# Kernel tuning notes

Measured on AMD Instinct MI355X. Metric: run time of the kernel, lower is better.

The kernel has to match this reference:

```python
import jax, jax.numpy as jnp
import numpy as np

N = 100000   # nodes
E = 1600000  # edges
IN, H1, H2, OUT = 512, 64, 16, 40


def setup_inputs() -> dict:
    key = jax.random.key(0)
    ks = jax.random.split(key, 8)
    x = jax.random.normal(ks[0], (N, IN), jnp.float32)
    edge_index = jax.random.randint(ks[1], (2, E), 0, N, dtype=jnp.int64)

    def glorot(k, i, o):
        s = np.sqrt(6.0 / (i + o)).astype(np.float32)
        return jax.random.uniform(k, (i, o), jnp.float32, -s, s)

    return dict(
        x=x, edge_index=edge_index,
        W1=glorot(ks[2], IN, H1), b1=jnp.zeros((H1,), jnp.float32),
        W2=glorot(ks[3], H1, H2), b2=jnp.zeros((H2,), jnp.float32),
        W3=glorot(ks[4], H2, OUT), b3=jnp.zeros((OUT,), jnp.float32),
    )


def _gcn_conv(x, src, dst, W, b):
    # PyG GCNConv: x' = D^{-1/2} (A + I) D^{-1/2} (x W) + b
    h = x @ W                                   # [N, F_out]
    n = x.shape[0]
    deg = jnp.zeros((n,), h.dtype).at[dst].add(1.0) + 1.0   # self-loop adds 1
    dinv = jax.lax.rsqrt(deg)                   # deg >= 1 always
    norm = dinv[src] * dinv[dst]                # [E]
    msg = h[src] * norm[:, None]                # gather + scale  [E, F_out]
    out = jnp.zeros_like(h).at[dst].add(msg)    # scatter-add to targets
    out = out + h * (dinv * dinv)[:, None]      # self-loop contribution
    return out + b


def reference(x, edge_index, W1, b1, W2, b2, W3, b3):
    src, dst = edge_index[0], edge_index[1]
    h = jax.nn.relu(_gcn_conv(x, src, dst, W1, b1))
    # dropout(p=0.2, training=False) -> identity
    h = jax.nn.relu(_gcn_conv(h, src, dst, W2, b2))
    h = _gcn_conv(h, src, dst, W3, b3)
    return jax.nn.log_softmax(h, axis=-1)
```

## Files before the change

### kernel.cpp

```cpp
#include <hip/hip_runtime.h>
#include <cstdint>
#include <cstddef>

#define NNODES 100000
#define NEDGES 1600000
#define NWIN 100
#define WIN_NODES 1000
#define WCAP 17408
#define WSTR 16

#define GM_ROWS 128
#define APAD 72
#define GEMM_BLOCKS ((NNODES + GM_ROWS - 1) / GM_ROWS)
#define BUCKET_BLOCKS 512
#define BCHUNK ((NEDGES + BUCKET_BLOCKS - 1) / BUCKET_BLOCKS)
#define MEGA_BLOCKS (GEMM_BLOCKS + BUCKET_BLOCKS)

typedef __attribute__((ext_vector_type(8))) short bf16x8;
typedef __attribute__((ext_vector_type(4))) float f32x4;
typedef __attribute__((ext_vector_type(4))) unsigned short ushort4v;
typedef __attribute__((ext_vector_type(8))) unsigned short ushort8v;

__device__ inline unsigned short f2bf(float f) {
    union { float f; unsigned u; } v; v.f = f;
    unsigned r = v.u + 0x7FFFu + ((v.u >> 16) & 1u);
    return (unsigned short)(r >> 16);
}
__device__ inline float bf2f(unsigned short b) {
    union { unsigned u; float f; } v; v.u = ((unsigned)b) << 16; return v.f;
}
__device__ inline void bfpair(unsigned u, float& lo, float& hi) {
    union { unsigned x; float f; } a, b;
    a.x = u << 16; b.x = u & 0xffff0000u;
    lo = a.f; hi = b.f;
}


__global__ __launch_bounds__(256) void convW(const float* __restrict__ W,
                                             unsigned short* __restrict__ Wt,
                                             int* __restrict__ wcur) {
    if (blockIdx.x == 0 && threadIdx.x < NWIN) wcur[threadIdx.x * WSTR] = 0;
    int i = blockIdx.x * 256 + threadIdx.x;
    if (i < 512 * 64) {
        int k = i >> 6, n = i & 63;
        Wt[n * 512 + k] = f2bf(W[i]);
    }
}


__global__ __launch_bounds__(256) void mega_gemm_bucket(
        const float* __restrict__ A,
        const unsigned short* __restrict__ Wt,
        unsigned short* __restrict__ Hs,
        const int* __restrict__ src, const int* __restrict__ dst,
        unsigned* __restrict__ stage,
        int* __restrict__ wcur, int M, int E) {
    __shared__ __align__(16) unsigned char smem[18432 + 9216];

    long long b = blockIdx.x;
    int g0 = (int)((b * GEMM_BLOCKS) / MEGA_BLOCKS);
    int g1 = (int)(((b + 1) * GEMM_BLOCKS) / MEGA_BLOCKS);

    if (g1 > g0) {
        typedef unsigned short RowA[APAD];
        RowA* As = (RowA*)smem;
        RowA* Bs = (RowA*)(smem + 18432);
        const int tid = threadIdx.x;
        const int wid = tid >> 6;
        const int lane = tid & 63;
        const int bm = g0 * GM_ROWS;

        f32x4 acc[2][4];
#pragma unroll
        for (int i = 0; i < 2; i++)
#pragma unroll
            for (int j = 0; j < 4; j++) acc[i][j] = (f32x4){0.f, 0.f, 0.f, 0.f};

        const int ar = tid >> 4;
        const int ac4 = tid & 15;
        const int lm = lane & 15;
        const int lk = (lane >> 4) * 8;

        float4 aR0[8], aR1[8];
        ushort8v bR0[2], bR1[2];

        auto LOADA = [&](float4 (&aRx)[8], ushort8v (&bRx)[2], int k0) {
#pragma unroll
            for (int p = 0; p < 8; p++) {
                int row = bm + p * 16 + ar;
                if (row < M) aRx[p] = *(const float4*)&A[(size_t)row * 512 + k0 + ac4 * 4];
                else         aRx[p] = make_float4(0.f, 0.f, 0.f, 0.f);
            }
#pragma unroll
            for (int p = 0; p < 2; p++) {
                int c = p * 256 + tid;
                int n = c >> 3, kc = c & 7;
                bRx[p] = *(const ushort8v*)&Wt[(size_t)n * 512 + k0 + kc * 8];
            }
        };

        auto TILE = [&](float4 (&aRx)[8], ushort8v (&bRx)[2], int k0) {
#pragma unroll
            for (int p = 0; p < 8; p++) {
                int r = p * 16 + ar;
                unsigned lo, hi;
                asm("v_cvt_pk_bf16_f32 %0, %1, %2" : "=v"(lo) : "v"(aRx[p].x), "v"(aRx[p].y));
                asm("v_cvt_pk_bf16_f32 %0, %1, %2" : "=v"(hi) : "v"(aRx[p].z), "v"(aRx[p].w));
                uint2 u; u.x = lo; u.y = hi;
                *(uint2*)&As[r][ac4 * 4] = u;
            }
#pragma unroll
            for (int p = 0; p < 2; p++) {
                int c = p * 256 + tid;
                int n = c >> 3, kc = c & 7;
                *(ushort8v*)&Bs[n][kc * 8] = bRx[p];
            }
            __syncthreads();

            if (k0 + 128 < 512) LOADA(aRx, bRx, k0 + 128);

            bf16x8 a[2][2], bb[4][2];
#pragma unroll
            for (int rf = 0; rf < 2; rf++)
#pragma unroll
                for (int kf = 0; kf < 2; kf++)
                    a[rf][kf] = *(const bf16x8*)&As[wid * 32 + rf * 16 + lm][kf * 32 + lk];
#pragma unroll
            for (int cf = 0; cf < 4; cf++)
#pragma unroll
                for (int kf = 0; kf < 2; kf++)
                    bb[cf][kf] = *(const bf16x8*)&Bs[cf * 16 + lm][kf * 32 + lk];

            __builtin_amdgcn_s_setprio(1);
#pragma unroll
            for (int kf = 0; kf < 2; kf++)
#pragma unroll
                for (int rf = 0; rf < 2; rf++)
#pragma unroll
                    for (int cf = 0; cf < 4; cf++)
                        acc[rf][cf] = __builtin_amdgcn_mfma_f32_16x16x32_bf16(
                            a[rf][kf], bb[cf][kf], acc[rf][cf], 0, 0, 0);
            __builtin_amdgcn_s_setprio(0);
            __syncthreads();
        };

        LOADA(aR0, bR0, 0);
        LOADA(aR1, bR1, 64);
        for (int tp = 0; tp < 4; tp++) {
            TILE(aR0, bR0, tp * 128);
            TILE(aR1, bR1, tp * 128 + 64);
        }

#pragma unroll
        for (int rf = 0; rf < 2; rf++) {
#pragma unroll
            for (int j = 0; j < 4; j++) {
                int row = bm + wid * 32 + rf * 16 + (lane >> 4) * 4 + j;
                if (row < M) {
#pragma unroll
                    for (int cf = 0; cf < 4; cf++)
                        Hs[(size_t)row * 64 + cf * 16 + lm] = f2bf(acc[rf][cf][j]);
                }
            }
        }
    } else {
        int bi = (int)(b - g0);
        int* cnt  = (int*)smem;
        int* lcur = cnt + NWIN;
        const int tid = threadIdx.x;
        int e0 = bi * BCHUNK;
        int e1 = e0 + BCHUNK; if (e1 > E) e1 = E;

        for (int i = tid; i < NWIN; i += 256) cnt[i] = 0;
        __syncthreads();
        for (int e = e0 + tid; e < e1; e += 256) {
            int d = dst[e];
            atomicAdd(&cnt[d / WIN_NODES], 1);
        }
        __syncthreads();
        for (int i = tid; i < NWIN; i += 256)
            lcur[i] = atomicAdd(&wcur[i * WSTR], cnt[i]);
        __syncthreads();
        for (int e = e0 + tid; e < e1; e += 256) {
            int d = dst[e], s = src[e];
            int w = d / WIN_NODES;
            int pos = atomicAdd(&lcur[w], 1);
            if (pos < WCAP)
                stage[(size_t)w * WCAP + pos] =
                    ((unsigned)(d - w * WIN_NODES) << 17) | (unsigned)s;
        }
    }
}


__global__ __launch_bounds__(256) void csr_window(
        const unsigned* __restrict__ stage,
        const int* __restrict__ wcur,
        int* __restrict__ rowstart,
        float* __restrict__ dinv,
        int* __restrict__ csr) {
    __shared__ int cnt[WIN_NODES];
    __shared__ int red[256];
    const int w = blockIdx.x;
    const int t = threadIdx.x;
    const int wb = w * WIN_NODES;
    const size_t sb = (size_t)w * WCAP;

    int v = (t < w) ? min(wcur[t * WSTR], WCAP) : 0;
    red[t] = v;
    __syncthreads();
#pragma unroll
    for (int off = 128; off > 0; off >>= 1) {
        if (t < off) red[t] += red[t + off];
        __syncthreads();
    }
    int woff = red[0];
    int n_w = min(wcur[w * WSTR], WCAP);
    __syncthreads();

    for (int i = t; i < WIN_NODES; i += 256) cnt[i] = 0;
    __syncthreads();
    for (int i = t; i < n_w; i += 256)
        atomicAdd(&cnt[stage[sb + i] >> 17], 1);
    __syncthreads();

    int c0 = 0, c1 = 0, c2 = 0, c3 = 0, psum = 0;
    if (t < 250) {
        c0 = cnt[4 * t]; c1 = cnt[4 * t + 1]; c2 = cnt[4 * t + 2]; c3 = cnt[4 * t + 3];
        psum = c0 + c1 + c2 + c3;
    }
    red[t] = psum;
    __syncthreads();
#pragma unroll
    for (int off = 1; off < 256; off <<= 1) {
        int tv = (t >= off) ? red[t - off] : 0;
        __syncthreads();
        red[t] += tv;
        __syncthreads();
    }
    int excl = red[t] - psum;
    if (t < 250) {
        int running = woff + excl;
        int idx = 4 * t;
        rowstart[wb + idx] = running; dinv[wb + idx] = rsqrtf((float)c0 + 1.f);
        cnt[idx] = running; running += c0;
        rowstart[wb + idx + 1] = running; dinv[wb + idx + 1] = rsqrtf((float)c1 + 1.f);
        cnt[idx + 1] = running; running += c1;
        rowstart[wb + idx + 2] = running; dinv[wb + idx + 2] = rsqrtf((float)c2 + 1.f);
        cnt[idx + 2] = running; running += c2;
        rowstart[wb + idx + 3] = running; dinv[wb + idx + 3] = rsqrtf((float)c3 + 1.f);
        cnt[idx + 3] = running;
    }
    if (w == NWIN - 1 && t == 0) rowstart[NNODES] = woff + n_w;
    __syncthreads();

    for (int i = t; i < n_w; i += 256) {
        unsigned p = stage[sb + i];
        int dl = (int)(p >> 17);
        int s  = (int)(p & 0x1FFFFu);
        int pos = atomicAdd(&cnt[dl], 1);
        csr[pos] = s;
    }
}


__global__ __launch_bounds__(256) void gather64_l2(
        const int* __restrict__ rowstart, const int* __restrict__ csr,
        const float* __restrict__ dinv,
        const unsigned short* __restrict__ Hs1,
        const float* __restrict__ b1,
        const float* __restrict__ W2,
        unsigned short* __restrict__ Hs2,
        int M) {
    __shared__ float Ws2[64 * 16];
    __shared__ float b1s[64];
    __shared__ float srow[8][64];
    for (int i = threadIdx.x; i < 64 * 16; i += 256) Ws2[i] = W2[i];
    if (threadIdx.x < 64) b1s[threadIdx.x] = b1[threadIdx.x];
    __syncthreads();

    const int r = threadIdx.x >> 5;
    const int lf = threadIdx.x & 31;
    const int row = blockIdx.x * 8 + r;
    const bool rok = (row < M);

    float v0 = 0.f, v1 = 0.f;
    if (rok) {
        const unsigned* H32 = (const unsigned*)Hs1;
        int e0 = rowstart[row], e1 = rowstart[row + 1];
        float dd = dinv[row];
        float acc0, acc1;
        bfpair(H32[(size_t)row * 32 + lf], acc0, acc1);
        acc0 *= dd; acc1 *= dd;
        int e = e0;
        for (; e + 3 < e1; e += 4) {
            int s0 = csr[e], s1 = csr[e + 1], s2 = csr[e + 2], s3 = csr[e + 3];
            float w0 = dinv[s0], w1 = dinv[s1], w2 = dinv[s2], w3 = dinv[s3];
            unsigned u0 = H32[(size_t)s0 * 32 + lf];
            unsigned u1 = H32[(size_t)s1 * 32 + lf];
            unsigned u2 = H32[(size_t)s2 * 32 + lf];
            unsigned u3 = H32[(size_t)s3 * 32 + lf];
            float a, b;
            bfpair(u0, a, b); acc0 += w0 * a; acc1 += w0 * b;
            bfpair(u1, a, b); acc0 += w1 * a; acc1 += w1 * b;
            bfpair(u2, a, b); acc0 += w2 * a; acc1 += w2 * b;
            bfpair(u3, a, b); acc0 += w3 * a; acc1 += w3 * b;
        }
        for (; e < e1; e++) {
            int s0 = csr[e];
            float w0 = dinv[s0];
            unsigned u = H32[(size_t)s0 * 32 + lf];
            float a, b;
            bfpair(u, a, b); acc0 += w0 * a; acc1 += w0 * b;
        }
        v0 = fmaxf(acc0 * dd + b1s[2 * lf], 0.f);
        v1 = fmaxf(acc1 * dd + b1s[2 * lf + 1], 0.f);
    }
    float2 t2; t2.x = v0; t2.y = v1;
    *(float2*)&srow[r][2 * lf] = t2;
    __syncthreads();

    if (rok && lf < 16) {
        float acc = 0.f;
#pragma unroll
        for (int k4 = 0; k4 < 16; k4++) {
            float4 s4 = *(const float4*)&srow[r][k4 * 4];
            acc += s4.x * Ws2[(k4 * 4 + 0) * 16 + lf];
            acc += s4.y * Ws2[(k4 * 4 + 1) * 16 + lf];
            acc += s4.z * Ws2[(k4 * 4 + 2) * 16 + lf];
            acc += s4.w * Ws2[(k4 * 4 + 3) * 16 + lf];
        }
        acc *= dinv[row];
        float hi = __shfl_down(acc, 1, 64);
        if ((lf & 1) == 0) {
            unsigned p = (unsigned)f2bf(acc) | ((unsigned)f2bf(hi) << 16);
            ((unsigned*)Hs2)[(size_t)row * 8 + (lf >> 1)] = p;
        }
    }
}


template <int F, bool RELU, bool SCALEOUT, bool HASBIAS, bool OUTBF>
__global__ __launch_bounds__(256) void gather_bf(
        const int* __restrict__ rowstart,
        const int* __restrict__ csr,
        const float* __restrict__ dinv,
        const unsigned short* __restrict__ Hs,
        const float* __restrict__ bias,
        void* __restrict__ outp,
        int M) {
    constexpr int LANES = F / 2;
    constexpr int GP = 256 / LANES;
    int row = blockIdx.x * GP + threadIdx.x / LANES;
    int lf = threadIdx.x % LANES;
    if (row >= M) return;

    const unsigned* H32 = (const unsigned*)Hs;
    const size_t LP = F / 2;

    int e0 = rowstart[row], e1 = rowstart[row + 1];
    float acc0, acc1;
    bfpair(H32[(size_t)row * LP + lf], acc0, acc1);

    int e = e0;
    for (; e + 3 < e1; e += 4) {
        int s0 = csr[e], s1 = csr[e + 1], s2 = csr[e + 2], s3 = csr[e + 3];
        unsigned u0 = H32[(size_t)s0 * LP + lf];
        unsigned u1 = H32[(size_t)s1 * LP + lf];
        unsigned u2 = H32[(size_t)s2 * LP + lf];
        unsigned u3 = H32[(size_t)s3 * LP + lf];
        float a, b;
        bfpair(u0, a, b); acc0 += a; acc1 += b;
        bfpair(u1, a, b); acc0 += a; acc1 += b;
        bfpair(u2, a, b); acc0 += a; acc1 += b;
        bfpair(u3, a, b); acc0 += a; acc1 += b;
    }
    for (; e < e1; e++) {
        unsigned u = H32[(size_t)csr[e] * LP + lf];
        float a, b;
        bfpair(u, a, b); acc0 += a; acc1 += b;
    }

    float dd = dinv[row];
    float v0 = acc0 * dd, v1 = acc1 * dd;
    if (HASBIAS) { v0 += bias[2 * lf]; v1 += bias[2 * lf + 1]; }
    if (RELU) { v0 = fmaxf(v0, 0.f); v1 = fmaxf(v1, 0.f); }
    if (SCALEOUT) { v0 *= dd; v1 *= dd; }
    if (OUTBF) {
        unsigned p = (unsigned)f2bf(v0) | ((unsigned)f2bf(v1) << 16);
        ((unsigned*)outp)[(size_t)row * LP + lf] = p;
    } else {
        float2 t; t.x = v0; t.y = v1;
        ((float2*)outp)[(size_t)row * LP + lf] = t;
    }
}


#define SRP 20

__global__ __launch_bounds__(256) void gather16_final(
        const int* __restrict__ rowstart, const int* __restrict__ csr,
        const float* __restrict__ dinv,
        const unsigned short* __restrict__ r2s,
        const float* __restrict__ W3,
        const float* __restrict__ b3,
        float* __restrict__ out,
        int M) {
    __shared__ float Ws3[16 * 40];
    __shared__ float bs3[40];
    __shared__ float srow[32][SRP];
    __shared__ float orow[32 * 40];
    for (int i = threadIdx.x; i < 16 * 40; i += 256) Ws3[i] = W3[i];
    if (threadIdx.x < 40) bs3[threadIdx.x] = b3[threadIdx.x];

    const int r = threadIdx.x >> 3;
    const int lf = threadIdx.x & 7;
    const int row = blockIdx.x * 32 + r;
    const bool rok = (row < M);

    float g0 = 0.f, g1 = 0.f;
    if (rok) {
        const unsigned* H32 = (const unsigned*)r2s;
        int e0 = rowstart[row], e1 = rowstart[row + 1];
        float acc0, acc1;
        bfpair(H32[(size_t)row * 8 + lf], acc0, acc1);
        int e = e0;
        for (; e + 3 < e1; e += 4) {
            int s0 = csr[e], s1 = csr[e + 1], s2 = csr[e + 2], s3 = csr[e + 3];
            unsigned u0 = H32[(size_t)s0 * 8 + lf];
            unsigned u1 = H32[(size_t)s1 * 8 + lf];
            unsigned u2 = H32[(size_t)s2 * 8 + lf];
            unsigned u3 = H32[(size_t)s3 * 8 + lf];
            float a, b;
            bfpair(u0, a, b); acc0 += a; acc1 += b;
            bfpair(u1, a, b); acc0 += a; acc1 += b;
            bfpair(u2, a, b); acc0 += a; acc1 += b;
            bfpair(u3, a, b); acc0 += a; acc1 += b;
        }
        for (; e < e1; e++) {
            unsigned u = H32[(size_t)csr[e] * 8 + lf];
            float a, b;
            bfpair(u, a, b); acc0 += a; acc1 += b;
        }
        float dd = dinv[row];
        g0 = acc0 * dd; g1 = acc1 * dd;
    }
    float2 t2; t2.x = g0; t2.y = g1;
    *(float2*)&srow[r][2 * lf] = t2;
    __syncthreads();

    float vals[5];
#pragma unroll
    for (int q = 0; q < 5; q++) vals[q] = bs3[lf + 8 * q];
#pragma unroll
    for (int k4 = 0; k4 < 4; k4++) {
        float4 s4 = *(const float4*)&srow[r][k4 * 4];
#pragma unroll
        for (int q = 0; q < 5; q++) {
            int n = lf + 8 * q;
            vals[q] += s4.x * Ws3[(k4 * 4 + 0) * 40 + n];
            vals[q] += s4.y * Ws3[(k4 * 4 + 1) * 40 + n];
            vals[q] += s4.z * Ws3[(k4 * 4 + 2) * 40 + n];
            vals[q] += s4.w * Ws3[(k4 * 4 + 3) * 40 + n];
        }
    }
    float m = vals[0];
#pragma unroll
    for (int q = 1; q < 5; q++) m = fmaxf(m, vals[q]);
#pragma unroll
    for (int off = 1; off < 8; off <<= 1) m = fmaxf(m, __shfl_xor(m, off, 64));
    float s = 0.f;
#pragma unroll
    for (int q = 0; q < 5; q++) s += expf(vals[q] - m);
#pragma unroll
    for (int off = 1; off < 8; off <<= 1) s += __shfl_xor(s, off, 64);
    float ls = logf(s) + m;
#pragma unroll
    for (int q = 0; q < 5; q++) orow[r * 40 + lf + 8 * q] = vals[q] - ls;
    __syncthreads();

    float4* o4 = (float4*)(out + (size_t)blockIdx.x * 32 * 40);
    const float4* s4p = (const float4*)orow;
    for (int i = threadIdx.x; i < 320; i += 256) {
        int rr = (i * 4) / 40;
        if (blockIdx.x * 32 + rr < M) o4[i] = s4p[i];
    }
}


extern "C" void kernel_launch(void* const* d_in, const int* in_sizes, int n_in,
                              void* d_out, int out_size, void* d_ws, size_t ws_size,
                              hipStream_t stream) {
    const float* x   = (const float*)d_in[0];
    const int*   ei  = (const int*)d_in[1];
    const int*   src = ei;
    const int*   dst = ei + NEDGES;
    const float* W1 = (const float*)d_in[2];
    const float* b1 = (const float*)d_in[3];
    const float* W2 = (const float*)d_in[4];
    const float* b2 = (const float*)d_in[5];
    const float* W3 = (const float*)d_in[6];
    const float* b3 = (const float*)d_in[7];
    float* out = (float*)d_out;

    int* ws_i = (int*)d_ws;
    int* wcur     = ws_i;
    int* rowstart = wcur + NWIN * WSTR + 16;
    int* csr      = rowstart + NNODES + 8;
    unsigned* stage = (unsigned*)(csr + NEDGES);
    float* dinv   = (float*)(stage + (size_t)NWIN * WCAP);
    unsigned short* Wt = (unsigned short*)(dinv + NNODES);
    float* bufA   = (float*)((int*)(Wt + 64 * 512) + 16);
    float* bufB   = bufA + (size_t)NNODES * 64;

    unsigned short* Hs1 = (unsigned short*)bufA;
    unsigned short* Hs2 = (unsigned short*)bufB;
    unsigned short* r2s = (unsigned short*)bufA;

    convW<<<(512 * 64 + 255) / 256, 256, 0, stream>>>(W1, Wt, wcur);

    mega_gemm_bucket<<<MEGA_BLOCKS, 256, 0, stream>>>(
        x, Wt, Hs1, src, dst, stage, wcur, NNODES, NEDGES);

    csr_window<<<NWIN, 256, 0, stream>>>(stage, wcur, rowstart, dinv, csr);

    gather64_l2<<<(NNODES + 7) / 8, 256, 0, stream>>>(
        rowstart, csr, dinv, Hs1, b1, W2, Hs2, NNODES);

    gather_bf<16, true, true, true, true><<<(NNODES + 31) / 32, 256, 0, stream>>>(
        rowstart, csr, dinv, Hs2, b2, r2s, NNODES);

    gather16_final<<<(NNODES + 31) / 32, 256, 0, stream>>>(
        rowstart, csr, dinv, r2s, W3, b3, out, NNODES);
}
```

Baseline: 201.5 us.

## Prescale layer-1 features by dinv in CSR build and widen gather loads

The CSR window kernel now also rescales each node's layer-1 bf16 feature row by its own dinv, so the first gather no longer loads dinv[src] per edge. All three gather kernels switch to 8-byte-per-lane loads with fewer lanes per row, more rows per block, and an 8-way unrolled edge loop, which cuts lane count and raises memory-level parallelism. The trade-offs are an extra read-modify-write pass over the 64-wide features and an additional bf16 rounding step.

```diff
diff --git a/kernel.cpp b/kernel.cpp
--- a/kernel.cpp
+++ b/kernel.cpp
@@ -198,8 +198,10 @@
         const int* __restrict__ wcur,
         int* __restrict__ rowstart,
         float* __restrict__ dinv,
-        int* __restrict__ csr) {
+        int* __restrict__ csr,
+        unsigned* __restrict__ H32) {
     __shared__ int cnt[WIN_NODES];
+    __shared__ float dlds[WIN_NODES];
     __shared__ int red[256];
     const int w = blockIdx.x;
     const int t = threadIdx.x;
@@ -242,13 +244,15 @@
     if (t < 250) {
         int running = woff + excl;
         int idx = 4 * t;
-        rowstart[wb + idx] = running; dinv[wb + idx] = rsqrtf((float)c0 + 1.f);
+        float d0 = rsqrtf((float)c0 + 1.f), d1 = rsqrtf((float)c1 + 1.f);
+        float d2 = rsqrtf((float)c2 + 1.f), d3 = rsqrtf((float)c3 + 1.f);
+        rowstart[wb + idx] = running; dinv[wb + idx] = d0; dlds[idx] = d0;
         cnt[idx] = running; running += c0;
-        rowstart[wb + idx + 1] = running; dinv[wb + idx + 1] = rsqrtf((float)c1 + 1.f);
+        rowstart[wb + idx + 1] = running; dinv[wb + idx + 1] = d1; dlds[idx + 1] = d1;
         cnt[idx + 1] = running; running += c1;
-        rowstart[wb + idx + 2] = running; dinv[wb + idx + 2] = rsqrtf((float)c2 + 1.f);
+        rowstart[wb + idx + 2] = running; dinv[wb + idx + 2] = d2; dlds[idx + 2] = d2;
         cnt[idx + 2] = running; running += c2;
-        rowstart[wb + idx + 3] = running; dinv[wb + idx + 3] = rsqrtf((float)c3 + 1.f);
+        rowstart[wb + idx + 3] = running; dinv[wb + idx + 3] = d3; dlds[idx + 3] = d3;
         cnt[idx + 3] = running;
     }
     if (w == NWIN - 1 && t == 0) rowstart[NNODES] = woff + n_w;
@@ -260,6 +264,16 @@
         int s  = (int)(p & 0x1FFFFu);
         int pos = atomicAdd(&cnt[dl], 1);
         csr[pos] = s;
+    }
+
+    for (int i = t; i < WIN_NODES * 32; i += 256) {
+        int dl = i >> 5;
+        float dd = dlds[dl];
+        size_t idx = (size_t)(wb + dl) * 32 + (i & 31);
+        unsigned u = H32[idx];
+        float lo, hi;
+        bfpair(u, lo, hi);
+        H32[idx] = (unsigned)f2bf(lo * dd) | ((unsigned)f2bf(hi * dd) << 16);
     }
 }
 
@@ -274,53 +288,61 @@
         int M) {
     __shared__ float Ws2[64 * 16];
     __shared__ float b1s[64];
-    __shared__ float srow[8][64];
+    __shared__ float srow[16][68];
     for (int i = threadIdx.x; i < 64 * 16; i += 256) Ws2[i] = W2[i];
     if (threadIdx.x < 64) b1s[threadIdx.x] = b1[threadIdx.x];
     __syncthreads();
 
-    const int r = threadIdx.x >> 5;
-    const int lf = threadIdx.x & 31;
-    const int row = blockIdx.x * 8 + r;
+    const int r = threadIdx.x >> 4;
+    const int lf = threadIdx.x & 15;
+    const int row = blockIdx.x * 16 + r;
     const bool rok = (row < M);
 
-    float v0 = 0.f, v1 = 0.f;
+    float a0 = 0.f, a1 = 0.f, a2 = 0.f, a3 = 0.f;
     if (rok) {
-        const unsigned* H32 = (const unsigned*)Hs1;
+        const uint2* H8 = (const uint2*)Hs1;
         int e0 = rowstart[row], e1 = rowstart[row + 1];
+        uint2 u = H8[(size_t)row * 16 + lf];
+        bfpair(u.x, a0, a1); bfpair(u.y, a2, a3);
+        int e = e0;
+        for (; e + 7 < e1; e += 8) {
+            int s0 = csr[e], s1 = csr[e+1], s2 = csr[e+2], s3 = csr[e+3];
+            int s4 = csr[e+4], s5 = csr[e+5], s6 = csr[e+6], s7 = csr[e+7];
+            uint2 u0 = H8[(size_t)s0 * 16 + lf];
+            uint2 u1 = H8[(size_t)s1 * 16 + lf];
+            uint2 u2 = H8[(size_t)s2 * 16 + lf];
+            uint2 u3 = H8[(size_t)s3 * 16 + lf];
+            uint2 u4 = H8[(size_t)s4 * 16 + lf];
+            uint2 u5 = H8[(size_t)s5 * 16 + lf];
+            uint2 u6 = H8[(size_t)s6 * 16 + lf];
+            uint2 u7 = H8[(size_t)s7 * 16 + lf];
+            float x0, x1;
+            bfpair(u0.x, x0, x1); a0 += x0; a1 += x1; bfpair(u0.y, x0, x1); a2 += x0; a3 += x1;
+            bfpair(u1.x, x0, x1); a0 += x0; a1 += x1; bfpair(u1.y, x0, x1); a2 += x0; a3 += x1;
+            bfpair(u2.x, x0, x1); a0 += x0; a1 += x1; bfpair(u2.y, x0, x1); a2 += x0; a3 += x1;
+            bfpair(u3.x, x0, x1); a0 += x0; a1 += x1; bfpair(u3.y, x0, x1); a2 += x0; a3 += x1;
+            bfpair(u4.x, x0, x1); a0 += x0; a1 += x1; bfpair(u4.y, x0, x1); a2 += x0; a3 += x1;
+            bfpair(u5.x, x0, x1); a0 += x0; a1 += x1; bfpair(u5.y, x0, x1); a2 += x0; a3 += x1;
+            bfpair(u6.x, x0, x1); a0 += x0; a1 += x1; bfpair(u6.y, x0, x1); a2 += x0; a3 += x1;
+            bfpair(u7.x, x0, x1); a0 += x0; a1 += x1; bfpair(u7.y, x0, x1); a2 += x0; a3 += x1;
+        }
+        for (; e < e1; e++) {
+            uint2 ue = H8[(size_t)csr[e] * 16 + lf];
+            float x0, x1;
+            bfpair(ue.x, x0, x1); a0 += x0; a1 += x1;
+            bfpair(ue.y, x0, x1); a2 += x0; a3 += x1;
+        }
         float dd = dinv[row];
-        float acc0, acc1;
-        bfpair(H32[(size_t)row * 32 + lf], acc0, acc1);
-        acc0 *= dd; acc1 *= dd;
-        int e = e0;
-        for (; e + 3 < e1; e += 4) {
-            int s0 = csr[e], s1 = csr[e + 1], s2 = csr[e + 2], s3 = csr[e + 3];
-            float w0 = dinv[s0], w1 = dinv[s1], w2 = dinv[s2], w3 = dinv[s3];
-            unsigned u0 = H32[(size_t)s0 * 32 + lf];
-            unsigned u1 = H32[(size_t)s1 * 32 + lf];
-            unsigned u2 = H32[(size_t)s2 * 32 + lf];
-            unsigned u3 = H32[(size_t)s3 * 32 + lf];
-            float a, b;
-            bfpair(u0, a, b); acc0 += w0 * a; acc1 += w0 * b;
-            bfpair(u1, a, b); acc0 += w1 * a; acc1 += w1 * b;
-            bfpair(u2, a, b); acc0 += w2 * a; acc1 += w2 * b;
-            bfpair(u3, a, b); acc0 += w3 * a; acc1 += w3 * b;
-        }
-        for (; e < e1; e++) {
-            int s0 = csr[e];
-            float w0 = dinv[s0];
-            unsigned u = H32[(size_t)s0 * 32 + lf];
-            float a, b;
-            bfpair(u, a, b); acc0 += w0 * a; acc1 += w0 * b;
-        }
-        v0 = fmaxf(acc0 * dd + b1s[2 * lf], 0.f);
-        v1 = fmaxf(acc1 * dd + b1s[2 * lf + 1], 0.f);
-    }
-    float2 t2; t2.x = v0; t2.y = v1;
-    *(float2*)&srow[r][2 * lf] = t2;
-    __syncthreads();
-
-    if (rok && lf < 16) {
+        a0 = fmaxf(a0 * dd + b1s[4 * lf + 0], 0.f);
+        a1 = fmaxf(a1 * dd + b1s[4 * lf + 1], 0.f);
+        a2 = fmaxf(a2 * dd + b1s[4 * lf + 2], 0.f);
+        a3 = fmaxf(a3 * dd + b1s[4 * lf + 3], 0.f);
+    }
+    float4 t4; t4.x = a0; t4.y = a1; t4.z = a2; t4.w = a3;
+    *(float4*)&srow[r][4 * lf] = t4;
+    __syncthreads();
+
+    if (rok) {
         float acc = 0.f;
 #pragma unroll
         for (int k4 = 0; k4 < 16; k4++) {
@@ -340,63 +362,75 @@
 }
 
 
-template <int F, bool RELU, bool SCALEOUT, bool HASBIAS, bool OUTBF>
-__global__ __launch_bounds__(256) void gather_bf(
-        const int* __restrict__ rowstart,
-        const int* __restrict__ csr,
+__global__ __launch_bounds__(256) void gather16_agg(
+        const int* __restrict__ rowstart, const int* __restrict__ csr,
         const float* __restrict__ dinv,
         const unsigned short* __restrict__ Hs,
         const float* __restrict__ bias,
-        void* __restrict__ outp,
+        unsigned short* __restrict__ outp,
         int M) {
-    constexpr int LANES = F / 2;
-    constexpr int GP = 256 / LANES;
-    int row = blockIdx.x * GP + threadIdx.x / LANES;
-    int lf = threadIdx.x % LANES;
+    __shared__ float bs[16];
+    if (threadIdx.x < 16) bs[threadIdx.x] = bias[threadIdx.x];
+    __syncthreads();
+
+    const int r = threadIdx.x >> 2;
+    const int lf = threadIdx.x & 3;
+    const int row = blockIdx.x * 64 + r;
     if (row >= M) return;
 
-    const unsigned* H32 = (const unsigned*)Hs;
-    const size_t LP = F / 2;
-
+    const unsigned long long* H8 = (const unsigned long long*)Hs;
     int e0 = rowstart[row], e1 = rowstart[row + 1];
-    float acc0, acc1;
-    bfpair(H32[(size_t)row * LP + lf], acc0, acc1);
-
+    unsigned long long u = H8[(size_t)row * 4 + lf];
+    float a0, a1, a2, a3;
+    bfpair((unsigned)u, a0, a1); bfpair((unsigned)(u >> 32), a2, a3);
     int e = e0;
-    for (; e + 3 < e1; e += 4) {
-        int s0 = csr[e], s1 = csr[e + 1], s2 = csr[e + 2], s3 = csr[e + 3];
-        unsigned u0 = H32[(size_t)s0 * LP + lf];
-        unsigned u1 = H32[(size_t)s1 * LP + lf];
-        unsigned u2 = H32[(size_t)s2 * LP + lf];
-        unsigned u3 = H32[(size_t)s3 * LP + lf];
-        float a, b;
-        bfpair(u0, a, b); acc0 += a; acc1 += b;
-        bfpair(u1, a, b); acc0 += a; acc1 += b;
-        bfpair(u2, a, b); acc0 += a; acc1 += b;
-        bfpair(u3, a, b); acc0 += a; acc1 += b;
+    for (; e + 7 < e1; e += 8) {
+        int s0 = csr[e], s1 = csr[e+1], s2 = csr[e+2], s3 = csr[e+3];
+        int s4 = csr[e+4], s5 = csr[e+5], s6 = csr[e+6], s7 = csr[e+7];
+        unsigned long long u0 = H8[(size_t)s0 * 4 + lf];
+        unsigned long long u1 = H8[(size_t)s1 * 4 + lf];
+        unsigned long long u2 = H8[(size_t)s2 * 4 + lf];
+        unsigned long long u3 = H8[(size_t)s3 * 4 + lf];
+        unsigned long long u4 = H8[(size_t)s4 * 4 + lf];
+        unsigned long long u5 = H8[(size_t)s5 * 4 + lf];
+        unsigned long long u6 = H8[(size_t)s6 * 4 + lf];
+        unsigned long long u7 = H8[(size_t)s7 * 4 + lf];
+        float x0, x1;
+        bfpair((unsigned)u0, x0, x1); a0 += x0; a1 += x1;
+        bfpair((unsigned)(u0 >> 32), x0, x1); a2 += x0; a3 += x1;
+        bfpair((unsigned)u1, x0, x1); a0 += x0; a1 += x1;
+        bfpair((unsigned)(u1 >> 32), x0, x1); a2 += x0; a3 += x1;
+        bfpair((unsigned)u2, x0, x1); a0 += x0; a1 += x1;
+        bfpair((unsigned)(u2 >> 32), x0, x1); a2 += x0; a3 += x1;
+        bfpair((unsigned)u3, x0, x1); a0 += x0; a1 += x1;
+        bfpair((unsigned)(u3 >> 32), x0, x1); a2 += x0; a3 += x1;
+        bfpair((unsigned)u4, x0, x1); a0 += x0; a1 += x1;
+        bfpair((unsigned)(u4 >> 32), x0, x1); a2 += x0; a3 += x1;
+        bfpair((unsigned)u5, x0, x1); a0 += x0; a1 += x1;
+        bfpair((unsigned)(u5 >> 32), x0, x1); a2 += x0; a3 += x1;
+        bfpair((unsigned)u6, x0, x1); a0 += x0; a1 += x1;
+        bfpair((unsigned)(u6 >> 32), x0, x1); a2 += x0; a3 += x1;
+        bfpair((unsigned)u7, x0, x1); a0 += x0; a1 += x1;
+        bfpair((unsigned)(u7 >> 32), x0, x1); a2 += x0; a3 += x1;
     }
     for (; e < e1; e++) {
-        unsigned u = H32[(size_t)csr[e] * LP + lf];
-        float a, b;
-        bfpair(u, a, b); acc0 += a; acc1 += b;
+        unsigned long long ue = H8[(size_t)csr[e] * 4 + lf];
+        float x0, x1;
+        bfpair((unsigned)ue, x0, x1); a0 += x0; a1 += x1;
+        bfpair((unsigned)(ue >> 32), x0, x1); a2 += x0; a3 += x1;
     }
 
     float dd = dinv[row];
-    float v0 = acc0 * dd, v1 = acc1 * dd;
-    if (HASBIAS) { v0 += bias[2 * lf]; v1 += bias[2 * lf + 1]; }
-    if (RELU) { v0 = fmaxf(v0, 0.f); v1 = fmaxf(v1, 0.f); }
-    if (SCALEOUT) { v0 *= dd; v1 *= dd; }
-    if (OUTBF) {
-        unsigned p = (unsigned)f2bf(v0) | ((unsigned)f2bf(v1) << 16);
-        ((unsigned*)outp)[(size_t)row * LP + lf] = p;
-    } else {
-        float2 t; t.x = v0; t.y = v1;
-        ((float2*)outp)[(size_t)row * LP + lf] = t;
-    }
-}
-
-
-#define SRP 20
+    a0 = fmaxf(a0 * dd + bs[4 * lf + 0], 0.f) * dd;
+    a1 = fmaxf(a1 * dd + bs[4 * lf + 1], 0.f) * dd;
+    a2 = fmaxf(a2 * dd + bs[4 * lf + 2], 0.f) * dd;
+    a3 = fmaxf(a3 * dd + bs[4 * lf + 3], 0.f) * dd;
+    uint2 p;
+    p.x = (unsigned)f2bf(a0) | ((unsigned)f2bf(a1) << 16);
+    p.y = (unsigned)f2bf(a2) | ((unsigned)f2bf(a3) << 16);
+    ((uint2*)outp)[(size_t)row * 4 + lf] = p;
+}
+
 
 __global__ __launch_bounds__(256) void gather16_final(
         const int* __restrict__ rowstart, const int* __restrict__ csr,
@@ -408,56 +442,74 @@
         int M) {
     __shared__ float Ws3[16 * 40];
     __shared__ float bs3[40];
-    __shared__ float srow[32][SRP];
-    __shared__ float orow[32 * 40];
+    __shared__ float srow[64][20];
+    __shared__ float orow[64 * 40];
     for (int i = threadIdx.x; i < 16 * 40; i += 256) Ws3[i] = W3[i];
     if (threadIdx.x < 40) bs3[threadIdx.x] = b3[threadIdx.x];
 
-    const int r = threadIdx.x >> 3;
-    const int lf = threadIdx.x & 7;
-    const int row = blockIdx.x * 32 + r;
+    const int r = threadIdx.x >> 2;
+    const int lf = threadIdx.x & 3;
+    const int row = blockIdx.x * 64 + r;
     const bool rok = (row < M);
 
-    float g0 = 0.f, g1 = 0.f;
+    float a0 = 0.f, a1 = 0.f, a2 = 0.f, a3 = 0.f;
     if (rok) {
-        const unsigned* H32 = (const unsigned*)r2s;
+        const unsigned long long* H8 = (const unsigned long long*)r2s;
         int e0 = rowstart[row], e1 = rowstart[row + 1];
-        float acc0, acc1;
-        bfpair(H32[(size_t)row * 8 + lf], acc0, acc1);
+        unsigned long long u = H8[(size_t)row * 4 + lf];
+        bfpair((unsigned)u, a0, a1); bfpair((unsigned)(u >> 32), a2, a3);
         int e = e0;
-        for (; e + 3 < e1; e += 4) {
-            int s0 = csr[e], s1 = csr[e + 1], s2 = csr[e + 2], s3 = csr[e + 3];
-            unsigned u0 = H32[(size_t)s0 * 8 + lf];
-            unsigned u1 = H32[(size_t)s1 * 8 + lf];
-            unsigned u2 = H32[(size_t)s2 * 8 + lf];
-            unsigned u3 = H32[(size_t)s3 * 8 + lf];
-            float a, b;
-            bfpair(u0, a, b); acc0 += a; acc1 += b;
-            bfpair(u1, a, b); acc0 += a; acc1 += b;
-            bfpair(u2, a, b); acc0 += a; acc1 += b;
-            bfpair(u3, a, b); acc0 += a; acc1 += b;
+        for (; e + 7 < e1; e += 8) {
+            int s0 = csr[e], s1 = csr[e+1], s2 = csr[e+2], s3 = csr[e+3];
+            int s4 = csr[e+4], s5 = csr[e+5], s6 = csr[e+6], s7 = csr[e+7];
+            unsigned long long u0 = H8[(size_t)s0 * 4 + lf];
+            unsigned long long u1 = H8[(size_t)s1 * 4 + lf];
+            unsigned long long u2 = H8[(size_t)s2 * 4 + lf];
+            unsigned long long u3 = H8[(size_t)s3 * 4 + lf];
+            unsigned long long u4 = H8[(size_t)s4 * 4 + lf];
+            unsigned long long u5 = H8[(size_t)s5 * 4 + lf];
+            unsigned long long u6 = H8[(size_t)s6 * 4 + lf];
+            unsigned long long u7 = H8[(size_t)s7 * 4 + lf];
+            float x0, x1;
+            bfpair((unsigned)u0, x0, x1); a0 += x0; a1 += x1;
+            bfpair((unsigned)(u0 >> 32), x0, x1); a2 += x0; a3 += x1;
+            bfpair((unsigned)u1, x0, x1); a0 += x0; a1 += x1;
+            bfpair((unsigned)(u1 >> 32), x0, x1); a2 += x0; a3 += x1;
+            bfpair((unsigned)u2, x0, x1); a0 += x0; a1 += x1;
+            bfpair((unsigned)(u2 >> 32), x0, x1); a2 += x0; a3 += x1;
+            bfpair((unsigned)u3, x0, x1); a0 += x0; a1 += x1;
+            bfpair((unsigned)(u3 >> 32), x0, x1); a2 += x0; a3 += x1;
+            bfpair((unsigned)u4, x0, x1); a0 += x0; a1 += x1;
+            bfpair((unsigned)(u4 >> 32), x0, x1); a2 += x0; a3 += x1;
+            bfpair((unsigned)u5, x0, x1); a0 += x0; a1 += x1;
+            bfpair((unsigned)(u5 >> 32), x0, x1); a2 += x0; a3 += x1;
+            bfpair((unsigned)u6, x0, x1); a0 += x0; a1 += x1;
+            bfpair((unsigned)(u6 >> 32), x0, x1); a2 += x0; a3 += x1;
+            bfpair((unsigned)u7, x0, x1); a0 += x0; a1 += x1;
+            bfpair((unsigned)(u7 >> 32), x0, x1); a2 += x0; a3 += x1;
         }
         for (; e < e1; e++) {
-            unsigned u = H32[(size_t)csr[e] * 8 + lf];
-            float a, b;
-            bfpair(u, a, b); acc0 += a; acc1 += b;
+            unsigned long long ue = H8[(size_t)csr[e] * 4 + lf];
+            float x0, x1;
+            bfpair((unsigned)ue, x0, x1); a0 += x0; a1 += x1;
+            bfpair((unsigned)(ue >> 32), x0, x1); a2 += x0; a3 += x1;
         }
         float dd = dinv[row];
-        g0 = acc0 * dd; g1 = acc1 * dd;
-    }
-    float2 t2; t2.x = g0; t2.y = g1;
-    *(float2*)&srow[r][2 * lf] = t2;
-    __syncthreads();
-
-    float vals[5];
-#pragma unroll
-    for (int q = 0; q < 5; q++) vals[q] = bs3[lf + 8 * q];
+        a0 *= dd; a1 *= dd; a2 *= dd; a3 *= dd;
+    }
+    float4 t4; t4.x = a0; t4.y = a1; t4.z = a2; t4.w = a3;
+    *(float4*)&srow[r][4 * lf] = t4;
+    __syncthreads();
+
+    float vals[10];
+#pragma unroll
+    for (int q = 0; q < 10; q++) vals[q] = bs3[lf + 4 * q];
 #pragma unroll
     for (int k4 = 0; k4 < 4; k4++) {
         float4 s4 = *(const float4*)&srow[r][k4 * 4];
 #pragma unroll
-        for (int q = 0; q < 5; q++) {
-            int n = lf + 8 * q;
+        for (int q = 0; q < 10; q++) {
+            int n = lf + 4 * q;
             vals[q] += s4.x * Ws3[(k4 * 4 + 0) * 40 + n];
             vals[q] += s4.y * Ws3[(k4 * 4 + 1) * 40 + n];
             vals[q] += s4.z * Ws3[(k4 * 4 + 2) * 40 + n];
@@ -466,24 +518,24 @@
     }
     float m = vals[0];
 #pragma unroll
-    for (int q = 1; q < 5; q++) m = fmaxf(m, vals[q]);
-#pragma unroll
-    for (int off = 1; off < 8; off <<= 1) m = fmaxf(m, __shfl_xor(m, off, 64));
+    for (int q = 1; q < 10; q++) m = fmaxf(m, vals[q]);
+#pragma unroll
+    for (int off = 1; off < 4; off <<= 1) m = fmaxf(m, __shfl_xor(m, off, 64));
     float s = 0.f;
 #pragma unroll
-    for (int q = 0; q < 5; q++) s += expf(vals[q] - m);
-#pragma unroll
-    for (int off = 1; off < 8; off <<= 1) s += __shfl_xor(s, off, 64);
+    for (int q = 0; q < 10; q++) s += expf(vals[q] - m);
+#pragma unroll
+    for (int off = 1; off < 4; off <<= 1) s += __shfl_xor(s, off, 64);
     float ls = logf(s) + m;
 #pragma unroll
-    for (int q = 0; q < 5; q++) orow[r * 40 + lf + 8 * q] = vals[q] - ls;
-    __syncthreads();
-
-    float4* o4 = (float4*)(out + (size_t)blockIdx.x * 32 * 40);
+    for (int q = 0; q < 10; q++) orow[r * 40 + lf + 4 * q] = vals[q] - ls;
+    __syncthreads();
+
+    float4* o4 = (float4*)(out + (size_t)blockIdx.x * 64 * 40);
     const float4* s4p = (const float4*)orow;
-    for (int i = threadIdx.x; i < 320; i += 256) {
+    for (int i = threadIdx.x; i < 640; i += 256) {
         int rr = (i * 4) / 40;
-        if (blockIdx.x * 32 + rr < M) o4[i] = s4p[i];
+        if (blockIdx.x * 64 + rr < M) o4[i] = s4p[i];
     }
 }
 
@@ -522,14 +574,15 @@
     mega_gemm_bucket<<<MEGA_BLOCKS, 256, 0, stream>>>(
         x, Wt, Hs1, src, dst, stage, wcur, NNODES, NEDGES);
 
-    csr_window<<<NWIN, 256, 0, stream>>>(stage, wcur, rowstart, dinv, csr);
-
-    gather64_l2<<<(NNODES + 7) / 8, 256, 0, stream>>>(
+    csr_window<<<NWIN, 256, 0, stream>>>(stage, wcur, rowstart, dinv, csr,
+                                         (unsigned*)Hs1);
+
+    gather64_l2<<<(NNODES + 15) / 16, 256, 0, stream>>>(
         rowstart, csr, dinv, Hs1, b1, W2, Hs2, NNODES);
 
-    gather_bf<16, true, true, true, true><<<(NNODES + 31) / 32, 256, 0, stream>>>(
+    gather16_agg<<<(NNODES + 63) / 64, 256, 0, stream>>>(
         rowstart, csr, dinv, Hs2, b2, r2s, NNODES);
 
-    gather16_final<<<(NNODES + 31) / 32, 256, 0, stream>>>(
+    gather16_final<<<(NNODES + 63) / 64, 256, 0, stream>>>(
         rowstart, csr, dinv, r2s, W3, b3, out, NNODES);
 }
```

Measured after the change: 209.5 us. 1.04x slower.

## Load GEMM operands directly into MFMA registers, dropping LDS staging

Applied to the files above, without the earlier changes.

The first-layer GEMM no longer stages A and W tiles through shared memory with barriers. Each lane now reads its fp32 rows of x straight from global memory, converts them to bf16 in registers, and loads the W fragments from global/L2 directly before issuing the MFMAs. This removes LDS traffic, the __syncthreads and the LDS footprint, which can raise occupancy. In exchange it loses the explicit double-buffered prefetch and uses less coalesced per-lane global loads of x and repeated W reads.

```diff
diff --git a/kernel.cpp b/kernel.cpp
--- a/kernel.cpp
+++ b/kernel.cpp
@@ -10,7 +10,6 @@
 #define WSTR 16
 
 #define GM_ROWS 128
-#define APAD 72
 #define GEMM_BLOCKS ((NNODES + GM_ROWS - 1) / GM_ROWS)
 #define BUCKET_BLOCKS 512
 #define BCHUNK ((NEDGES + BUCKET_BLOCKS - 1) / BUCKET_BLOCKS)
@@ -18,16 +17,11 @@
 
 typedef __attribute__((ext_vector_type(8))) short bf16x8;
 typedef __attribute__((ext_vector_type(4))) float f32x4;
-typedef __attribute__((ext_vector_type(4))) unsigned short ushort4v;
-typedef __attribute__((ext_vector_type(8))) unsigned short ushort8v;
 
 __device__ inline unsigned short f2bf(float f) {
     union { float f; unsigned u; } v; v.f = f;
     unsigned r = v.u + 0x7FFFu + ((v.u >> 16) & 1u);
     return (unsigned short)(r >> 16);
-}
-__device__ inline float bf2f(unsigned short b) {
-    union { unsigned u; float f; } v; v.u = ((unsigned)b) << 16; return v.f;
 }
 __device__ inline void bfpair(unsigned u, float& lo, float& hi) {
     union { unsigned x; float f; } a, b;
@@ -55,100 +49,64 @@
         const int* __restrict__ src, const int* __restrict__ dst,
         unsigned* __restrict__ stage,
         int* __restrict__ wcur, int M, int E) {
-    __shared__ __align__(16) unsigned char smem[18432 + 9216];
+    __shared__ int smem_cnt[NWIN];
+    __shared__ int smem_lcur[NWIN];
 
     long long b = blockIdx.x;
     int g0 = (int)((b * GEMM_BLOCKS) / MEGA_BLOCKS);
     int g1 = (int)(((b + 1) * GEMM_BLOCKS) / MEGA_BLOCKS);
 
     if (g1 > g0) {
-        typedef unsigned short RowA[APAD];
-        RowA* As = (RowA*)smem;
-        RowA* Bs = (RowA*)(smem + 18432);
         const int tid = threadIdx.x;
         const int wid = tid >> 6;
         const int lane = tid & 63;
-        const int bm = g0 * GM_ROWS;
-
-        f32x4 acc[2][4];
-#pragma unroll
-        for (int i = 0; i < 2; i++)
-#pragma unroll
-            for (int j = 0; j < 4; j++) acc[i][j] = (f32x4){0.f, 0.f, 0.f, 0.f};
-
-        const int ar = tid >> 4;
-        const int ac4 = tid & 15;
         const int lm = lane & 15;
         const int lk = (lane >> 4) * 8;
-
-        float4 aR0[8], aR1[8];
-        ushort8v bR0[2], bR1[2];
-
-        auto LOADA = [&](float4 (&aRx)[8], ushort8v (&bRx)[2], int k0) {
-#pragma unroll
-            for (int p = 0; p < 8; p++) {
-                int row = bm + p * 16 + ar;
-                if (row < M) aRx[p] = *(const float4*)&A[(size_t)row * 512 + k0 + ac4 * 4];
-                else         aRx[p] = make_float4(0.f, 0.f, 0.f, 0.f);
+        const int bm = g0 * GM_ROWS;
+
+        f32x4 acc[2][4];
+#pragma unroll
+        for (int i = 0; i < 2; i++)
+#pragma unroll
+            for (int j = 0; j < 4; j++) acc[i][j] = (f32x4){0.f, 0.f, 0.f, 0.f};
+
+        int row0 = bm + wid * 32 + lm;
+        int row1 = row0 + 16;
+        const float* p0 = &A[(size_t)min(row0, M - 1) * 512 + lk];
+        const float* p1 = &A[(size_t)min(row1, M - 1) * 512 + lk];
+
+#pragma unroll 2
+        for (int k0 = 0; k0 < 512; k0 += 32) {
+            float4 q00 = *(const float4*)(p0 + k0);
+            float4 q01 = *(const float4*)(p0 + k0 + 4);
+            float4 q10 = *(const float4*)(p1 + k0);
+            float4 q11 = *(const float4*)(p1 + k0 + 4);
+
+            unsigned af0[4], af1[4];
+            asm("v_cvt_pk_bf16_f32 %0, %1, %2" : "=v"(af0[0]) : "v"(q00.x), "v"(q00.y));
+            asm("v_cvt_pk_bf16_f32 %0, %1, %2" : "=v"(af0[1]) : "v"(q00.z), "v"(q00.w));
+            asm("v_cvt_pk_bf16_f32 %0, %1, %2" : "=v"(af0[2]) : "v"(q01.x), "v"(q01.y));
+            asm("v_cvt_pk_bf16_f32 %0, %1, %2" : "=v"(af0[3]) : "v"(q01.z), "v"(q01.w));
+            asm("v_cvt_pk_bf16_f32 %0, %1, %2" : "=v"(af1[0]) : "v"(q10.x), "v"(q10.y));
+            asm("v_cvt_pk_bf16_f32 %0, %1, %2" : "=v"(af1[1]) : "v"(q10.z), "v"(q10.w));
+            asm("v_cvt_pk_bf16_f32 %0, %1, %2" : "=v"(af1[2]) : "v"(q11.x), "v"(q11.y));
+            asm("v_cvt_pk_bf16_f32 %0, %1, %2" : "=v"(af1[3]) : "v"(q11.z), "v"(q11.w));
+            bf16x8 a0, a1;
+            a0 = *(bf16x8*)af0;
+            a1 = *(bf16x8*)af1;
+
+            bf16x8 bf[4];
+#pragma unroll
+            for (int cf = 0; cf < 4; cf++)
+                bf[cf] = *(const bf16x8*)&Wt[(size_t)(cf * 16 + lm) * 512 + k0 + lk];
+
+            __builtin_amdgcn_s_setprio(1);
+#pragma unroll
+            for (int cf = 0; cf < 4; cf++) {
+                acc[0][cf] = __builtin_amdgcn_mfma_f32_16x16x32_bf16(a0, bf[cf], acc[0][cf], 0, 0, 0);
+                acc[1][cf] = __builtin_amdgcn_mfma_f32_16x16x32_bf16(a1, bf[cf], acc[1][cf], 0, 0, 0);
             }
-#pragma unroll
-            for (int p = 0; p < 2; p++) {
-                int c = p * 256 + tid;
-                int n = c >> 3, kc = c & 7;
-                bRx[p] = *(const ushort8v*)&Wt[(size_t)n * 512 + k0 + kc * 8];
-            }
-        };
-
-        auto TILE = [&](float4 (&aRx)[8], ushort8v (&bRx)[2], int k0) {
-#pragma unroll
-            for (int p = 0; p < 8; p++) {
-                int r = p * 16 + ar;
-                unsigned lo, hi;
-                asm("v_cvt_pk_bf16_f32 %0, %1, %2" : "=v"(lo) : "v"(aRx[p].x), "v"(aRx[p].y));
-                asm("v_cvt_pk_bf16_f32 %0, %1, %2" : "=v"(hi) : "v"(aRx[p].z), "v"(aRx[p].w));
-                uint2 u; u.x = lo; u.y = hi;
-                *(uint2*)&As[r][ac4 * 4] = u;
-            }
-#pragma unroll
-            for (int p = 0; p < 2; p++) {
-                int c = p * 256 + tid;
-                int n = c >> 3, kc = c & 7;
-                *(ushort8v*)&Bs[n][kc * 8] = bRx[p];
-            }
-            __syncthreads();
-
-            if (k0 + 128 < 512) LOADA(aRx, bRx, k0 + 128);
-
-            bf16x8 a[2][2], bb[4][2];
-#pragma unroll
-            for (int rf = 0; rf < 2; rf++)
-#pragma unroll
-                for (int kf = 0; kf < 2; kf++)
-                    a[rf][kf] = *(const bf16x8*)&As[wid * 32 + rf * 16 + lm][kf * 32 + lk];
-#pragma unroll
-            for (int cf = 0; cf < 4; cf++)
-#pragma unroll
-                for (int kf = 0; kf < 2; kf++)
-                    bb[cf][kf] = *(const bf16x8*)&Bs[cf * 16 + lm][kf * 32 + lk];
-
-            __builtin_amdgcn_s_setprio(1);
-#pragma unroll
-            for (int kf = 0; kf < 2; kf++)
-#pragma unroll
-                for (int rf = 0; rf < 2; rf++)
-#pragma unroll
-                    for (int cf = 0; cf < 4; cf++)
-                        acc[rf][cf] = __builtin_amdgcn_mfma_f32_16x16x32_bf16(
-                            a[rf][kf], bb[cf][kf], acc[rf][cf], 0, 0, 0);
             __builtin_amdgcn_s_setprio(0);
-            __syncthreads();
-        };
-
-        LOADA(aR0, bR0, 0);
-        LOADA(aR1, bR1, 64);
-        for (int tp = 0; tp < 4; tp++) {
-            TILE(aR0, bR0, tp * 128);
-            TILE(aR1, bR1, tp * 128 + 64);
         }
 
 #pragma unroll
@@ -165,18 +123,16 @@
         }
     } else {
         int bi = (int)(b - g0);
-        int* cnt  = (int*)smem;
-        int* lcur = cnt + NWIN;
+        int* cnt  = smem_cnt;
+        int* lcur = smem_lcur;
         const int tid = threadIdx.x;
         int e0 = bi * BCHUNK;
         int e1 = e0 + BCHUNK; if (e1 > E) e1 = E;
 
         for (int i = tid; i < NWIN; i += 256) cnt[i] = 0;
         __syncthreads();
-        for (int e = e0 + tid; e < e1; e += 256) {
-            int d = dst[e];
-            atomicAdd(&cnt[d / WIN_NODES], 1);
-        }
+        for (int e = e0 + tid; e < e1; e += 256)
+            atomicAdd(&cnt[dst[e] / WIN_NODES], 1);
         __syncthreads();
         for (int i = tid; i < NWIN; i += 256)
             lcur[i] = atomicAdd(&wcur[i * WSTR], cnt[i]);
@@ -517,7 +473,7 @@
     unsigned short* Hs2 = (unsigned short*)bufB;
     unsigned short* r2s = (unsigned short*)bufA;
 
-    convW<<<(512 * 64 + 255) / 256, 256, 0, stream>>>(W1, Wt, wcur);
+    convW<<<128, 256, 0, stream>>>(W1, Wt, wcur);
 
     mega_gemm_bucket<<<MEGA_BLOCKS, 256, 0, stream>>>(
         x, Wt, Hs1, src, dst, stage, wcur, NNODES, NEDGES);
```

Result: slower. 233.9 us (+16.1%).
